# Kernel optimization log

Measured on AMD Instinct MI355X. Metric: run time of the kernel, lower is better.

## Reference

```python
import jax, jax.numpy as jnp
import numpy as np

BS, N, C = 16, 128, 512
EPS = 1e-5


def setup_inputs() -> dict:
    key = jax.random.key(0)
    ks = jax.random.split(key, 6)
    x = jax.random.normal(ks[0], (BS, N, C), dtype=jnp.float32)
    y = jax.random.normal(ks[1], (BS, C), dtype=jnp.float32)
    # edge conv: Conv2d(2C -> 1, 1x1), init std sqrt(2/(1*1*1))
    conv_e_w = jax.random.normal(ks[2], (1, 2 * C), dtype=jnp.float32) * np.sqrt(2.0)
    conv_e_b = jnp.zeros((1,), dtype=jnp.float32)
    bn_e_g = jnp.ones((1,), dtype=jnp.float32)
    bn_e_b = jnp.zeros((1,), dtype=jnp.float32)
    bn_e_m = jnp.zeros((1,), dtype=jnp.float32)
    bn_e_v = jnp.ones((1,), dtype=jnp.float32)
    # feature conv: Conv2d(2C -> C, 1x1), init std sqrt(2/C)
    conv_f_w = jax.random.normal(ks[3], (C, 2 * C), dtype=jnp.float32) * np.sqrt(2.0 / C)
    conv_f_b = jnp.zeros((C,), dtype=jnp.float32)
    bn_f_g = jnp.ones((C,), dtype=jnp.float32)
    bn_f_b = jnp.zeros((C,), dtype=jnp.float32)
    bn_f_m = jnp.zeros((C,), dtype=jnp.float32)
    bn_f_v = jnp.ones((C,), dtype=jnp.float32)
    return {
        "x": x, "y": y,
        "conv_e_w": conv_e_w, "conv_e_b": conv_e_b,
        "bn_e_g": bn_e_g, "bn_e_b": bn_e_b, "bn_e_m": bn_e_m, "bn_e_v": bn_e_v,
        "conv_f_w": conv_f_w, "conv_f_b": conv_f_b,
        "bn_f_g": bn_f_g, "bn_f_b": bn_f_b, "bn_f_m": bn_f_m, "bn_f_v": bn_f_v,
    }


def reference(x, y, conv_e_w, conv_e_b, bn_e_g, bn_e_b, bn_e_m, bn_e_v,
              conv_f_w, conv_f_b, bn_f_g, bn_f_b, bn_f_m, bn_f_v):
    bs, n, c = x.shape
    # ---- Wcompute: pairwise |x_i - x_j| -> conv1x1(2C->1) + BN + mask + softmax ----
    diff = jnp.abs(x[:, :, None, :] - x[:, None, :, :])  # [bs, N, N, C]
    w_diff = conv_e_w[0, :c]   # weights on pairwise-diff channels
    w_y = conv_e_w[0, c:]      # weights on broadcast y channels
    # 1x1 conv collapses to einsum; y part is constant over (i, j)
    score = (jnp.einsum('bijc,c->bij', diff, w_diff)
             + (y @ w_y)[:, None, None] + conv_e_b[0])  # [bs, N, N]
    # BatchNorm2d(1), inference mode
    score = (score - bn_e_m[0]) * (bn_e_g[0] * jax.lax.rsqrt(bn_e_v[0] + EPS)) + bn_e_b[0]
    # mask diagonal (W_id * 1e8) then softmax over neighbors j
    score = score - jnp.eye(n, dtype=score.dtype)[None] * 1e8
    W = jax.nn.softmax(score, axis=2)  # [bs, N, N]
    # ---- Gconv: neighbor aggregation + conv1x1(2C->C) + BN + ReLU ----
    x_nb = jnp.einsum('bij,bjc->bic', W, x)       # [bs, N, C]
    h = jnp.concatenate([x, x_nb], axis=2)        # [bs, N, 2C]
    out = jnp.einsum('bnk,ck->bnc', h, conv_f_w) + conv_f_b  # [bs, N, C]
    # BatchNorm2d(C), inference mode (per-channel)
    out = (out - bn_f_m) * (bn_f_g * jax.lax.rsqrt(bn_f_v + EPS)) + bn_f_b
    return jax.nn.relu(out)
```

## Files before the change

### kernel.cpp

```cpp
#include <hip/hip_runtime.h>
#include <hip/hip_bf16.h>

#define NTOK 128
#define CHN  512
#define KTOT 1024
#define EPSV 1e-5f

typedef __attribute__((ext_vector_type(8))) short bf16x8;
typedef __attribute__((ext_vector_type(4))) float f32x4;

union BfPack4 { ushort4 u; __hip_bfloat16 h[4]; };


__global__ __launch_bounds__(256)
void k0_transpose(const float* __restrict__ xg,
                  float* __restrict__ xT,
                  __hip_bfloat16* __restrict__ xTbf,
                  __hip_bfloat16* __restrict__ hb)
{
    __shared__ float ts[64 * 68];
    const int t  = threadIdx.x;
    const int bk = blockIdx.x;
    const int b  = bk >> 4;
    const int jt = (bk >> 3) & 1;
    const int ct = bk & 7;
    const int j0 = jt * 64, c0 = ct * 64;

    const int jr = t >> 2, qd = t & 3;
    const float* src = xg + ((size_t)(b * NTOK) + j0 + jr) * CHN + c0 + qd * 16;
    float4 v0 = *(const float4*)&src[0];
    float4 v1 = *(const float4*)&src[4];
    float4 v2 = *(const float4*)&src[8];
    float4 v3 = *(const float4*)&src[12];
    *(float4*)&ts[jr * 68 + qd * 16 + 0]  = v0;
    *(float4*)&ts[jr * 68 + qd * 16 + 4]  = v1;
    *(float4*)&ts[jr * 68 + qd * 16 + 8]  = v2;
    *(float4*)&ts[jr * 68 + qd * 16 + 12] = v3;

    {
        __hip_bfloat16* hrow = hb + ((size_t)(b * NTOK) + j0 + jr) * KTOT + c0 + qd * 16;
        BfPack4 p;
        p.h[0]=__float2bfloat16(v0.x); p.h[1]=__float2bfloat16(v0.y);
        p.h[2]=__float2bfloat16(v0.z); p.h[3]=__float2bfloat16(v0.w);
        *(ushort4*)&hrow[0] = p.u;
        p.h[0]=__float2bfloat16(v1.x); p.h[1]=__float2bfloat16(v1.y);
        p.h[2]=__float2bfloat16(v1.z); p.h[3]=__float2bfloat16(v1.w);
        *(ushort4*)&hrow[4] = p.u;
        p.h[0]=__float2bfloat16(v2.x); p.h[1]=__float2bfloat16(v2.y);
        p.h[2]=__float2bfloat16(v2.z); p.h[3]=__float2bfloat16(v2.w);
        *(ushort4*)&hrow[8] = p.u;
        p.h[0]=__float2bfloat16(v3.x); p.h[1]=__float2bfloat16(v3.y);
        p.h[2]=__float2bfloat16(v3.z); p.h[3]=__float2bfloat16(v3.w);
        *(ushort4*)&hrow[12] = p.u;
    }
    __syncthreads();

    const int cs = t >> 4, jj = (t & 15) * 4;
    #pragma unroll
    for (int m = 0; m < 4; ++m) {
        const int c = cs + 16 * m;
        float4 o;
        o.x = ts[(jj + 0) * 68 + c];
        o.y = ts[(jj + 1) * 68 + c];
        o.z = ts[(jj + 2) * 68 + c];
        o.w = ts[(jj + 3) * 68 + c];
        const size_t base = ((size_t)(b * CHN) + c0 + c) * NTOK + j0 + jj;
        *(float4*)&xT[base] = o;
        BfPack4 p;
        p.h[0]=__float2bfloat16(o.x); p.h[1]=__float2bfloat16(o.y);
        p.h[2]=__float2bfloat16(o.z); p.h[3]=__float2bfloat16(o.w);
        *(ushort4*)&xTbf[base] = p.u;
    }
}

__global__ __launch_bounds__(128)
void k1a_scores(const float* __restrict__ xg,
                const float* __restrict__ xT,
                const float* __restrict__ wde,
                float* __restrict__ part)
{
    const int bk = blockIdx.x;
    const int s  = bk & 7;
    const int iq = (bk >> 3) & 31;
    const int b  = bk >> 8;
    const int i0 = iq * 4;
    const int c0 = s * 64;
    const int j  = threadIdx.x;

    const float* xtp = xT + ((size_t)(b * CHN) + c0) * NTOK + j;
    const float* xip = xg + ((size_t)(b * NTOK) + i0) * CHN + c0;

    float acc0 = 0.f, acc1 = 0.f, acc2 = 0.f, acc3 = 0.f;

    #pragma unroll 2
    for (int cc = 0; cc < 64; cc += 8) {
        float xj[8];
        #pragma unroll
        for (int k = 0; k < 8; ++k) xj[k] = xtp[(cc + k) * NTOK];
        #pragma unroll
        for (int k = 0; k < 8; ++k) {
            const int c = cc + k;
            const float wd  = wde[c0 + c];
            const float xi0 = xip[0 * CHN + c];
            const float xi1 = xip[1 * CHN + c];
            const float xi2 = xip[2 * CHN + c];
            const float xi3 = xip[3 * CHN + c];
            acc0 += fabsf(xi0 - xj[k]) * wd;
            acc1 += fabsf(xi1 - xj[k]) * wd;
            acc2 += fabsf(xi2 - xj[k]) * wd;
            acc3 += fabsf(xi3 - xj[k]) * wd;
        }
    }

    float* pp = part + ((size_t)s * 16 + b) * (NTOK * NTOK) + (size_t)i0 * NTOK + j;
    pp[0 * NTOK] = acc0;
    pp[1 * NTOK] = acc1;
    pp[2 * NTOK] = acc2;
    pp[3 * NTOK] = acc3;
}

__global__ __launch_bounds__(128)
void k1b_softmax(const float* __restrict__ part,
                 const float* __restrict__ bn_e_g,
                 const float* __restrict__ bn_e_v,
                 __hip_bfloat16* __restrict__ Wbf)
{
    const int bk = blockIdx.x;
    const int b  = bk >> 6;
    const int i  = (bk & 63) * 2 + (threadIdx.x >> 6);
    const int l  = threadIdx.x & 63;

    const float* pp = part + (size_t)(b * NTOK + i) * NTOK;
    float p1 = 0.f, p2 = 0.f;
    #pragma unroll
    for (int s = 0; s < 8; ++s) {
        p1 += pp[(size_t)s * 16 * NTOK * NTOK + l];
        p2 += pp[(size_t)s * 16 * NTOK * NTOK + l + 64];
    }
    const float sc = bn_e_g[0] * rsqrtf(bn_e_v[0] + EPSV);
    float l1 = p1 * sc - (l == i ? 1e8f : 0.f);
    float l2 = p2 * sc - (l + 64 == i ? 1e8f : 0.f);

    float m = fmaxf(l1, l2);
    #pragma unroll
    for (int off = 32; off > 0; off >>= 1) m = fmaxf(m, __shfl_xor(m, off));
    const float e1 = __expf(l1 - m);
    const float e2 = __expf(l2 - m);
    float ssum = e1 + e2;
    #pragma unroll
    for (int off = 32; off > 0; off >>= 1) ssum += __shfl_xor(ssum, off);
    const float inv = 1.f / ssum;

    __hip_bfloat16* wr = Wbf + (size_t)(b * NTOK + i) * NTOK;
    wr[l]      = __float2bfloat16(e1 * inv);
    wr[l + 64] = __float2bfloat16(e2 * inv);
}

__global__ __launch_bounds__(256)
void k1c_xnb(const __hip_bfloat16* __restrict__ Wbf,
             const __hip_bfloat16* __restrict__ xTbf,
             const float* __restrict__ wf,
             __hip_bfloat16* __restrict__ hb,
             __hip_bfloat16* __restrict__ wfb)
{
    const int bk = blockIdx.x;
    const int t  = threadIdx.x;

    {
        const float* wr = wf + (size_t)bk * KTOT;
        float4 u = *(const float4*)&wr[t * 4];
        BfPack4 p;
        p.h[0]=__float2bfloat16(u.x); p.h[1]=__float2bfloat16(u.y);
        p.h[2]=__float2bfloat16(u.z); p.h[3]=__float2bfloat16(u.w);
        *(ushort4*)&wfb[(size_t)bk * KTOT + t * 4] = p.u;
    }

    const int b  = bk >> 5;
    const int mt = (bk >> 3) & 3;
    const int ct = bk & 7;
    const int i0 = mt * 32, c0 = ct * 64;

    const int w    = t >> 6;
    const int lane = t & 63;
    const int wm   = w & 1;
    const int wn   = w >> 1;
    const int m16  = lane & 15;
    const int q    = lane >> 4;

    const short* A0 = (const short*)Wbf  + (size_t)(b * NTOK + i0 + wm * 16 + m16) * NTOK + q * 8;
    const short* B0 = (const short*)xTbf + ((size_t)(b * CHN) + c0 + wn * 32 + m16) * NTOK + q * 8;

    f32x4 acc0 = {0.f, 0.f, 0.f, 0.f};
    f32x4 acc1 = acc0;

    #pragma unroll
    for (int k0 = 0; k0 < NTOK; k0 += 32) {
        const bf16x8 a  = *(const bf16x8*)(A0 + k0);
        const bf16x8 b0 = *(const bf16x8*)(B0 + k0);
        const bf16x8 b1 = *(const bf16x8*)(B0 + 16 * NTOK + k0);
        acc0 = __builtin_amdgcn_mfma_f32_16x16x32_bf16(a, b0, acc0, 0, 0, 0);
        acc1 = __builtin_amdgcn_mfma_f32_16x16x32_bf16(a, b1, acc1, 0, 0, 0);
    }

    #pragma unroll
    for (int ni = 0; ni < 2; ++ni) {
        const int c = c0 + wn * 32 + ni * 16 + m16;
        const f32x4 ac = ni ? acc1 : acc0;
        #pragma unroll
        for (int r = 0; r < 4; ++r) {
            const int i = i0 + wm * 16 + q * 4 + r;
            hb[(size_t)(b * NTOK + i) * KTOT + CHN + c] = __float2bfloat16(ac[r]);
        }
    }
}

__global__ __launch_bounds__(256)
void k2_gemm_bn_relu(const __hip_bfloat16* __restrict__ hbp,
                     const __hip_bfloat16* __restrict__ wfbp,
                     const float* __restrict__ fb,
                     const float* __restrict__ gg,
                     const float* __restrict__ bb,
                     const float* __restrict__ mm,
                     const float* __restrict__ vv,
                     float* __restrict__ out)
{
    const int blk  = blockIdx.x;
    const int r0   = (blk >> 3) << 6;
    const int c0   = (blk & 7) << 6;
    const int t    = threadIdx.x;
    const int w    = t >> 6;
    const int lane = t & 63;
    const int wm   = w & 1;
    const int wn   = w >> 1;
    const int m16  = lane & 15;
    const int qq   = lane >> 4;

    const short* A0 = (const short*)hbp  + (size_t)(r0 + wm * 32 + m16) * KTOT + qq * 8;
    const short* B0 = (const short*)wfbp + (size_t)(c0 + wn * 32 + m16) * KTOT + qq * 8;

    f32x4 acc00 = {0.f, 0.f, 0.f, 0.f};
    f32x4 acc01 = acc00, acc10 = acc00, acc11 = acc00;

    #pragma unroll 4
    for (int k0 = 0; k0 < KTOT; k0 += 32) {
        const bf16x8 aA = *(const bf16x8*)(A0 + k0);
        const bf16x8 aB = *(const bf16x8*)(A0 + 16 * KTOT + k0);
        const bf16x8 bA = *(const bf16x8*)(B0 + k0);
        const bf16x8 bB = *(const bf16x8*)(B0 + 16 * KTOT + k0);
        acc00 = __builtin_amdgcn_mfma_f32_16x16x32_bf16(aA, bA, acc00, 0, 0, 0);
        acc01 = __builtin_amdgcn_mfma_f32_16x16x32_bf16(aA, bB, acc01, 0, 0, 0);
        acc10 = __builtin_amdgcn_mfma_f32_16x16x32_bf16(aB, bA, acc10, 0, 0, 0);
        acc11 = __builtin_amdgcn_mfma_f32_16x16x32_bf16(aB, bB, acc11, 0, 0, 0);
    }

    #pragma unroll
    for (int ni = 0; ni < 2; ++ni) {
        const int c = c0 + wn * 32 + ni * 16 + m16;
        const float gf = gg[c] * rsqrtf(vv[c] + EPSV);
        const float ad = fb[c] - mm[c];
        const float bv = bb[c];
        const f32x4 acr0 = ni ? acc01 : acc00;
        const f32x4 acr1 = ni ? acc11 : acc10;
        #pragma unroll
        for (int r2 = 0; r2 < 4; ++r2) {
            int row = r0 + wm * 32 + qq * 4 + r2;
            float val = (acr0[r2] + ad) * gf + bv;
            out[(size_t)row * CHN + c] = fmaxf(val, 0.f);
            row += 16;
            val = (acr1[r2] + ad) * gf + bv;
            out[(size_t)row * CHN + c] = fmaxf(val, 0.f);
        }
    }
}

extern "C" void kernel_launch(void* const* d_in, const int* in_sizes, int n_in,
                              void* d_out, int out_size, void* d_ws, size_t ws_size,
                              hipStream_t stream) {
    const float* x        = (const float*)d_in[0];
    const float* conv_e_w = (const float*)d_in[2];
    const float* bn_e_g   = (const float*)d_in[4];
    const float* bn_e_v   = (const float*)d_in[7];
    const float* conv_f_w = (const float*)d_in[8];
    const float* conv_f_b = (const float*)d_in[9];
    const float* bn_f_g   = (const float*)d_in[10];
    const float* bn_f_b   = (const float*)d_in[11];
    const float* bn_f_m   = (const float*)d_in[12];
    const float* bn_f_v   = (const float*)d_in[13];
    float* out = (float*)d_out;

    char* ws = (char*)d_ws;
    float*           xT   = (float*)(ws);
    float*           part = (float*)(ws + (4u << 20));
    __hip_bfloat16*  hb   = (__hip_bfloat16*)(ws + (12u << 20));
    __hip_bfloat16*  wfb  = (__hip_bfloat16*)(ws + (16u << 20));
    __hip_bfloat16*  Wbf  = (__hip_bfloat16*)(ws + (17u << 20));
    __hip_bfloat16*  xTbf = (__hip_bfloat16*)(ws + (17u << 20) + (512u << 10));

    k0_transpose<<<256, 256, 0, stream>>>(x, xT, xTbf, hb);
    k1a_scores<<<4096, 128, 0, stream>>>(x, xT, conv_e_w, part);
    k1b_softmax<<<1024, 128, 0, stream>>>(part, bn_e_g, bn_e_v, Wbf);
    k1c_xnb<<<512, 256, 0, stream>>>(Wbf, xTbf, conv_f_w, hb, wfb);
    k2_gemm_bn_relu<<<256, 256, 0, stream>>>(hb, wfb, conv_f_b, bn_f_g, bn_f_b,
                                             bn_f_m, bn_f_v, out);
}
```

Before: 123.1 us.

## Fuse softmax into neighbor GEMM and vectorize score kernel with channel-quad layout

The separate softmax kernel is merged into the neighbor-aggregation kernel. Each block reduces the partial scores for its 32 rows, computes the masked softmax and keeps the bf16 weights in shared memory instead of writing them to global memory and reading them back. The score kernel now processes 8 query rows per block and reads a new channel-quad interleaved transposed layout with float4 loads, which raises reuse per loaded x_j. In exchange, the fused kernel recomputes the softmax once per channel tile (8x redundant), and the transpose kernel now writes the bf16 transpose with scalar stores.

```diff
diff --git a/kernel.cpp b/kernel.cpp
--- a/kernel.cpp
+++ b/kernel.cpp
@@ -14,7 +14,7 @@
 
 __global__ __launch_bounds__(256)
 void k0_transpose(const float* __restrict__ xg,
-                  float* __restrict__ xT,
+                  float* __restrict__ xT4,
                   __hip_bfloat16* __restrict__ xTbf,
                   __hip_bfloat16* __restrict__ hb)
 {
@@ -55,114 +55,69 @@
     }
     __syncthreads();
 
-    const int cs = t >> 4, jj = (t & 15) * 4;
+    const int jr2 = t & 63;
     #pragma unroll
     for (int m = 0; m < 4; ++m) {
-        const int c = cs + 16 * m;
-        float4 o;
-        o.x = ts[(jj + 0) * 68 + c];
-        o.y = ts[(jj + 1) * 68 + c];
-        o.z = ts[(jj + 2) * 68 + c];
-        o.w = ts[(jj + 3) * 68 + c];
-        const size_t base = ((size_t)(b * CHN) + c0 + c) * NTOK + j0 + jj;
-        *(float4*)&xT[base] = o;
-        BfPack4 p;
-        p.h[0]=__float2bfloat16(o.x); p.h[1]=__float2bfloat16(o.y);
-        p.h[2]=__float2bfloat16(o.z); p.h[3]=__float2bfloat16(o.w);
-        *(ushort4*)&xTbf[base] = p.u;
+        const int cg = (t >> 6) * 4 + m;
+        float4 f4 = *(const float4*)&ts[jr2 * 68 + cg * 4];
+        const size_t slot = ((size_t)(b * 128) + (c0 >> 2) + cg) * NTOK + j0 + jr2;
+        *(float4*)&xT4[slot * 4] = f4;
+        const int c = c0 + cg * 4;
+        xTbf[((size_t)(b * CHN) + c + 0) * NTOK + j0 + jr2] = __float2bfloat16(f4.x);
+        xTbf[((size_t)(b * CHN) + c + 1) * NTOK + j0 + jr2] = __float2bfloat16(f4.y);
+        xTbf[((size_t)(b * CHN) + c + 2) * NTOK + j0 + jr2] = __float2bfloat16(f4.z);
+        xTbf[((size_t)(b * CHN) + c + 3) * NTOK + j0 + jr2] = __float2bfloat16(f4.w);
     }
 }
 
 __global__ __launch_bounds__(128)
 void k1a_scores(const float* __restrict__ xg,
-                const float* __restrict__ xT,
+                const float* __restrict__ xT4,
                 const float* __restrict__ wde,
                 float* __restrict__ part)
 {
     const int bk = blockIdx.x;
     const int s  = bk & 7;
-    const int iq = (bk >> 3) & 31;
-    const int b  = bk >> 8;
-    const int i0 = iq * 4;
+    const int iq = (bk >> 3) & 15;
+    const int b  = bk >> 7;
+    const int i0 = iq * 8;
     const int c0 = s * 64;
     const int j  = threadIdx.x;
 
-    const float* xtp = xT + ((size_t)(b * CHN) + c0) * NTOK + j;
+    const float* xt  = xT4 + ((size_t)(b * 128 + s * 16) * NTOK + j) * 4;
     const float* xip = xg + ((size_t)(b * NTOK) + i0) * CHN + c0;
 
-    float acc0 = 0.f, acc1 = 0.f, acc2 = 0.f, acc3 = 0.f;
-
-    #pragma unroll 2
-    for (int cc = 0; cc < 64; cc += 8) {
-        float xj[8];
-        #pragma unroll
-        for (int k = 0; k < 8; ++k) xj[k] = xtp[(cc + k) * NTOK];
-        #pragma unroll
-        for (int k = 0; k < 8; ++k) {
-            const int c = cc + k;
-            const float wd  = wde[c0 + c];
-            const float xi0 = xip[0 * CHN + c];
-            const float xi1 = xip[1 * CHN + c];
-            const float xi2 = xip[2 * CHN + c];
-            const float xi3 = xip[3 * CHN + c];
-            acc0 += fabsf(xi0 - xj[k]) * wd;
-            acc1 += fabsf(xi1 - xj[k]) * wd;
-            acc2 += fabsf(xi2 - xj[k]) * wd;
-            acc3 += fabsf(xi3 - xj[k]) * wd;
-        }
-    }
-
-    float* pp = part + ((size_t)s * 16 + b) * (NTOK * NTOK) + (size_t)i0 * NTOK + j;
-    pp[0 * NTOK] = acc0;
-    pp[1 * NTOK] = acc1;
-    pp[2 * NTOK] = acc2;
-    pp[3 * NTOK] = acc3;
-}
-
-__global__ __launch_bounds__(128)
-void k1b_softmax(const float* __restrict__ part,
-                 const float* __restrict__ bn_e_g,
-                 const float* __restrict__ bn_e_v,
-                 __hip_bfloat16* __restrict__ Wbf)
+    float acc[8];
+    #pragma unroll
+    for (int r = 0; r < 8; ++r) acc[r] = 0.f;
+
+    #pragma unroll 4
+    for (int g = 0; g < 16; ++g) {
+        const float4 xj = *(const float4*)(xt + (size_t)g * NTOK * 4);
+        const float4 wd = *(const float4*)&wde[c0 + g * 4];
+        #pragma unroll
+        for (int r = 0; r < 8; ++r) {
+            const float4 xi = *(const float4*)&xip[r * CHN + g * 4];
+            acc[r] += fabsf(xi.x - xj.x) * wd.x + fabsf(xi.y - xj.y) * wd.y
+                    + fabsf(xi.z - xj.z) * wd.z + fabsf(xi.w - xj.w) * wd.w;
+        }
+    }
+
+    float* pp = part + ((size_t)(s * 16 + b)) * (NTOK * NTOK) + (size_t)i0 * NTOK + j;
+    #pragma unroll
+    for (int r = 0; r < 8; ++r) pp[r * NTOK] = acc[r];
+}
+
+__global__ __launch_bounds__(256)
+void k1bc_softmax_xnb(const float* __restrict__ part,
+                      const float* __restrict__ bn_e_g,
+                      const float* __restrict__ bn_e_v,
+                      const __hip_bfloat16* __restrict__ xTbf,
+                      const float* __restrict__ wf,
+                      __hip_bfloat16* __restrict__ hb,
+                      __hip_bfloat16* __restrict__ wfb)
 {
-    const int bk = blockIdx.x;
-    const int b  = bk >> 6;
-    const int i  = (bk & 63) * 2 + (threadIdx.x >> 6);
-    const int l  = threadIdx.x & 63;
-
-    const float* pp = part + (size_t)(b * NTOK + i) * NTOK;
-    float p1 = 0.f, p2 = 0.f;
-    #pragma unroll
-    for (int s = 0; s < 8; ++s) {
-        p1 += pp[(size_t)s * 16 * NTOK * NTOK + l];
-        p2 += pp[(size_t)s * 16 * NTOK * NTOK + l + 64];
-    }
-    const float sc = bn_e_g[0] * rsqrtf(bn_e_v[0] + EPSV);
-    float l1 = p1 * sc - (l == i ? 1e8f : 0.f);
-    float l2 = p2 * sc - (l + 64 == i ? 1e8f : 0.f);
-
-    float m = fmaxf(l1, l2);
-    #pragma unroll
-    for (int off = 32; off > 0; off >>= 1) m = fmaxf(m, __shfl_xor(m, off));
-    const float e1 = __expf(l1 - m);
-    const float e2 = __expf(l2 - m);
-    float ssum = e1 + e2;
-    #pragma unroll
-    for (int off = 32; off > 0; off >>= 1) ssum += __shfl_xor(ssum, off);
-    const float inv = 1.f / ssum;
-
-    __hip_bfloat16* wr = Wbf + (size_t)(b * NTOK + i) * NTOK;
-    wr[l]      = __float2bfloat16(e1 * inv);
-    wr[l + 64] = __float2bfloat16(e2 * inv);
-}
-
-__global__ __launch_bounds__(256)
-void k1c_xnb(const __hip_bfloat16* __restrict__ Wbf,
-             const __hip_bfloat16* __restrict__ xTbf,
-             const float* __restrict__ wf,
-             __hip_bfloat16* __restrict__ hb,
-             __hip_bfloat16* __restrict__ wfb)
-{
+    __shared__ unsigned short WL[32 * 128];
     const int bk = blockIdx.x;
     const int t  = threadIdx.x;
 
@@ -180,6 +135,57 @@
     const int ct = bk & 7;
     const int i0 = mt * 32, c0 = ct * 64;
 
+    {
+        const int r    = t >> 3;
+        const int jseg = (t & 7) * 16;
+        const int gi   = i0 + r;
+
+        float4 s0 = {0,0,0,0}, s1 = s0, s2 = s0, s3 = s0;
+        #pragma unroll
+        for (int s = 0; s < 8; ++s) {
+            const float* pp = part + ((size_t)(s * 16 + b)) * (NTOK * NTOK)
+                            + (size_t)gi * NTOK + jseg;
+            float4 a = *(const float4*)&pp[0];
+            float4 bq = *(const float4*)&pp[4];
+            float4 cq = *(const float4*)&pp[8];
+            float4 dq = *(const float4*)&pp[12];
+            s0.x+=a.x; s0.y+=a.y; s0.z+=a.z; s0.w+=a.w;
+            s1.x+=bq.x; s1.y+=bq.y; s1.z+=bq.z; s1.w+=bq.w;
+            s2.x+=cq.x; s2.y+=cq.y; s2.z+=cq.z; s2.w+=cq.w;
+            s3.x+=dq.x; s3.y+=dq.y; s3.z+=dq.z; s3.w+=dq.w;
+        }
+        const float sc = bn_e_g[0] * rsqrtf(bn_e_v[0] + EPSV);
+        float l[16] = { s0.x,s0.y,s0.z,s0.w, s1.x,s1.y,s1.z,s1.w,
+                        s2.x,s2.y,s2.z,s2.w, s3.x,s3.y,s3.z,s3.w };
+        #pragma unroll
+        for (int k = 0; k < 16; ++k) l[k] *= sc;
+        if (gi >= jseg && gi < jseg + 16) l[gi - jseg] -= 1e8f;
+
+        float m = l[0];
+        #pragma unroll
+        for (int k = 1; k < 16; ++k) m = fmaxf(m, l[k]);
+        m = fmaxf(m, __shfl_xor(m, 1));
+        m = fmaxf(m, __shfl_xor(m, 2));
+        m = fmaxf(m, __shfl_xor(m, 4));
+        float e[16], ssum = 0.f;
+        #pragma unroll
+        for (int k = 0; k < 16; ++k) { e[k] = __expf(l[k] - m); ssum += e[k]; }
+        ssum += __shfl_xor(ssum, 1);
+        ssum += __shfl_xor(ssum, 2);
+        ssum += __shfl_xor(ssum, 4);
+        const float inv = 1.f / ssum;
+        #pragma unroll
+        for (int k4 = 0; k4 < 4; ++k4) {
+            BfPack4 p;
+            p.h[0] = __float2bfloat16(e[k4*4+0] * inv);
+            p.h[1] = __float2bfloat16(e[k4*4+1] * inv);
+            p.h[2] = __float2bfloat16(e[k4*4+2] * inv);
+            p.h[3] = __float2bfloat16(e[k4*4+3] * inv);
+            *(ushort4*)&WL[r * 128 + jseg + k4 * 4] = p.u;
+        }
+    }
+    __syncthreads();
+
     const int w    = t >> 6;
     const int lane = t & 63;
     const int wm   = w & 1;
@@ -187,7 +193,7 @@
     const int m16  = lane & 15;
     const int q    = lane >> 4;
 
-    const short* A0 = (const short*)Wbf  + (size_t)(b * NTOK + i0 + wm * 16 + m16) * NTOK + q * 8;
+    const unsigned short* A0 = &WL[(wm * 16 + m16) * 128 + q * 8];
     const short* B0 = (const short*)xTbf + ((size_t)(b * CHN) + c0 + wn * 32 + m16) * NTOK + q * 8;
 
     f32x4 acc0 = {0.f, 0.f, 0.f, 0.f};
@@ -289,17 +295,16 @@
     float* out = (float*)d_out;
 
     char* ws = (char*)d_ws;
-    float*           xT   = (float*)(ws);
-    float*           part = (float*)(ws + (4u << 20));
+    float*           xT4  = (float*)(ws);
+    float*           part = (float*)(ws + (4u  << 20));
     __hip_bfloat16*  hb   = (__hip_bfloat16*)(ws + (12u << 20));
     __hip_bfloat16*  wfb  = (__hip_bfloat16*)(ws + (16u << 20));
-    __hip_bfloat16*  Wbf  = (__hip_bfloat16*)(ws + (17u << 20));
-    __hip_bfloat16*  xTbf = (__hip_bfloat16*)(ws + (17u << 20) + (512u << 10));
-
-    k0_transpose<<<256, 256, 0, stream>>>(x, xT, xTbf, hb);
-    k1a_scores<<<4096, 128, 0, stream>>>(x, xT, conv_e_w, part);
-    k1b_softmax<<<1024, 128, 0, stream>>>(part, bn_e_g, bn_e_v, Wbf);
-    k1c_xnb<<<512, 256, 0, stream>>>(Wbf, xTbf, conv_f_w, hb, wfb);
+    __hip_bfloat16*  xTbf = (__hip_bfloat16*)(ws + (17u << 20));
+
+    k0_transpose<<<256, 256, 0, stream>>>(x, xT4, xTbf, hb);
+    k1a_scores<<<2048, 128, 0, stream>>>(x, xT4, conv_e_w, part);
+    k1bc_softmax_xnb<<<512, 256, 0, stream>>>(part, bn_e_g, bn_e_v, xTbf,
+                                              conv_f_w, hb, wfb);
     k2_gemm_bn_relu<<<256, 256, 0, stream>>>(hb, wfb, conv_f_b, bn_f_g, bn_f_b,
                                              bn_f_m, bn_f_v, out);
 }
```

New measurement: 138.4 us. 1.12x slower.

## Fuse neighbor aggregation into final GEMM and stage x tile in LDS for scores

Applied to the files above, without the earlier changes.

The scores kernel now loads a per-batch x channel slice into shared memory, transposed in place, instead of reading a global fp32 transpose. It also computes 8 rows per 256-thread block. The xT fp32 buffer and the separate x_nb kernel are removed. The final kernel recomputes W·x for its 64-row tile into LDS, then runs the concat GEMM from bf16 x and that LDS buffer. This removes one launch and the hb round trip, at the cost of redundant W·x work across the 8 column-tile blocks.

```diff
diff --git a/kernel.cpp b/kernel.cpp
--- a/kernel.cpp
+++ b/kernel.cpp
@@ -5,6 +5,7 @@
 #define CHN  512
 #define KTOT 1024
 #define EPSV 1e-5f
+#define XNB_LD 520
 
 typedef __attribute__((ext_vector_type(8))) short bf16x8;
 typedef __attribute__((ext_vector_type(4))) float f32x4;
@@ -13,10 +14,72 @@
 
 
 __global__ __launch_bounds__(256)
-void k0_transpose(const float* __restrict__ xg,
-                  float* __restrict__ xT,
-                  __hip_bfloat16* __restrict__ xTbf,
-                  __hip_bfloat16* __restrict__ hb)
+void k1a_scores(const float* __restrict__ xg,
+                const float* __restrict__ wde,
+                float* __restrict__ part)
+{
+    __shared__ float xs[64 * 129];
+    const int bk = blockIdx.x;
+    const int s  = bk & 7;
+    const int ib = (bk >> 3) & 15;
+    const int b  = bk >> 7;
+    const int i0 = ib * 8;
+    const int c0 = s * 64;
+    const int t  = threadIdx.x;
+    const float* __restrict__ xb = xg + (size_t)b * NTOK * CHN;
+
+    const int cq = t & 15, jb = t >> 4;
+    #pragma unroll
+    for (int u = 0; u < 8; ++u) {
+        const int j = jb + 16 * u;
+        float4 v = *(const float4*)&xb[(size_t)j * CHN + c0 + cq * 4];
+        xs[(cq * 4 + 0) * 129 + j] = v.x;
+        xs[(cq * 4 + 1) * 129 + j] = v.y;
+        xs[(cq * 4 + 2) * 129 + j] = v.z;
+        xs[(cq * 4 + 3) * 129 + j] = v.w;
+    }
+    __syncthreads();
+
+    const int j  = t & 127;
+    const int rh = t >> 7;
+    const float* xip = xb + (size_t)(i0 + rh * 4) * CHN + c0;
+
+    float acc[4] = {0.f, 0.f, 0.f, 0.f};
+    #pragma unroll 4
+    for (int g = 0; g < 16; ++g) {
+        const float4 wd  = *(const float4*)&wde[c0 + g * 4];
+        const float4 xi0 = *(const float4*)&xip[0 * CHN + g * 4];
+        const float4 xi1 = *(const float4*)&xip[1 * CHN + g * 4];
+        const float4 xi2 = *(const float4*)&xip[2 * CHN + g * 4];
+        const float4 xi3 = *(const float4*)&xip[3 * CHN + g * 4];
+        const float xj0 = xs[(g * 4 + 0) * 129 + j];
+        const float xj1 = xs[(g * 4 + 1) * 129 + j];
+        const float xj2 = xs[(g * 4 + 2) * 129 + j];
+        const float xj3 = xs[(g * 4 + 3) * 129 + j];
+        acc[0] += fabsf(xi0.x - xj0) * wd.x + fabsf(xi0.y - xj1) * wd.y
+                + fabsf(xi0.z - xj2) * wd.z + fabsf(xi0.w - xj3) * wd.w;
+        acc[1] += fabsf(xi1.x - xj0) * wd.x + fabsf(xi1.y - xj1) * wd.y
+                + fabsf(xi1.z - xj2) * wd.z + fabsf(xi1.w - xj3) * wd.w;
+        acc[2] += fabsf(xi2.x - xj0) * wd.x + fabsf(xi2.y - xj1) * wd.y
+                + fabsf(xi2.z - xj2) * wd.z + fabsf(xi2.w - xj3) * wd.w;
+        acc[3] += fabsf(xi3.x - xj0) * wd.x + fabsf(xi3.y - xj1) * wd.y
+                + fabsf(xi3.z - xj2) * wd.z + fabsf(xi3.w - xj3) * wd.w;
+    }
+
+    float* pp = part + ((size_t)s * 16 + b) * (NTOK * NTOK)
+              + (size_t)(i0 + rh * 4) * NTOK + j;
+    pp[0 * NTOK] = acc[0];
+    pp[1 * NTOK] = acc[1];
+    pp[2 * NTOK] = acc[2];
+    pp[3 * NTOK] = acc[3];
+}
+
+__global__ __launch_bounds__(256)
+void k0_prep(const float* __restrict__ xg,
+             const float* __restrict__ wf,
+             __hip_bfloat16* __restrict__ xbf,
+             __hip_bfloat16* __restrict__ xTbf,
+             __hip_bfloat16* __restrict__ wfb)
 {
     __shared__ float ts[64 * 68];
     const int t  = threadIdx.x;
@@ -25,6 +88,20 @@
     const int jt = (bk >> 3) & 1;
     const int ct = bk & 7;
     const int j0 = jt * 64, c0 = ct * 64;
+
+    {
+        const float* wr = wf + (size_t)(2 * bk) * KTOT;
+        __hip_bfloat16* wo = wfb + (size_t)(2 * bk) * KTOT;
+        #pragma unroll
+        for (int u = 0; u < 2; ++u) {
+            const int idx = t + u * 256;
+            float4 v = *(const float4*)&wr[idx * 4];
+            BfPack4 p;
+            p.h[0]=__float2bfloat16(v.x); p.h[1]=__float2bfloat16(v.y);
+            p.h[2]=__float2bfloat16(v.z); p.h[3]=__float2bfloat16(v.w);
+            *(ushort4*)&wo[idx * 4] = p.u;
+        }
+    }
 
     const int jr = t >> 2, qd = t & 3;
     const float* src = xg + ((size_t)(b * NTOK) + j0 + jr) * CHN + c0 + qd * 16;
@@ -38,7 +115,7 @@
     *(float4*)&ts[jr * 68 + qd * 16 + 12] = v3;
 
     {
-        __hip_bfloat16* hrow = hb + ((size_t)(b * NTOK) + j0 + jr) * KTOT + c0 + qd * 16;
+        __hip_bfloat16* hrow = xbf + ((size_t)(b * NTOK) + j0 + jr) * CHN + c0 + qd * 16;
         BfPack4 p;
         p.h[0]=__float2bfloat16(v0.x); p.h[1]=__float2bfloat16(v0.y);
         p.h[2]=__float2bfloat16(v0.z); p.h[3]=__float2bfloat16(v0.w);
@@ -59,64 +136,13 @@
     #pragma unroll
     for (int m = 0; m < 4; ++m) {
         const int c = cs + 16 * m;
-        float4 o;
-        o.x = ts[(jj + 0) * 68 + c];
-        o.y = ts[(jj + 1) * 68 + c];
-        o.z = ts[(jj + 2) * 68 + c];
-        o.w = ts[(jj + 3) * 68 + c];
-        const size_t base = ((size_t)(b * CHN) + c0 + c) * NTOK + j0 + jj;
-        *(float4*)&xT[base] = o;
         BfPack4 p;
-        p.h[0]=__float2bfloat16(o.x); p.h[1]=__float2bfloat16(o.y);
-        p.h[2]=__float2bfloat16(o.z); p.h[3]=__float2bfloat16(o.w);
-        *(ushort4*)&xTbf[base] = p.u;
-    }
-}
-
-__global__ __launch_bounds__(128)
-void k1a_scores(const float* __restrict__ xg,
-                const float* __restrict__ xT,
-                const float* __restrict__ wde,
-                float* __restrict__ part)
-{
-    const int bk = blockIdx.x;
-    const int s  = bk & 7;
-    const int iq = (bk >> 3) & 31;
-    const int b  = bk >> 8;
-    const int i0 = iq * 4;
-    const int c0 = s * 64;
-    const int j  = threadIdx.x;
-
-    const float* xtp = xT + ((size_t)(b * CHN) + c0) * NTOK + j;
-    const float* xip = xg + ((size_t)(b * NTOK) + i0) * CHN + c0;
-
-    float acc0 = 0.f, acc1 = 0.f, acc2 = 0.f, acc3 = 0.f;
-
-    #pragma unroll 2
-    for (int cc = 0; cc < 64; cc += 8) {
-        float xj[8];
-        #pragma unroll
-        for (int k = 0; k < 8; ++k) xj[k] = xtp[(cc + k) * NTOK];
-        #pragma unroll
-        for (int k = 0; k < 8; ++k) {
-            const int c = cc + k;
-            const float wd  = wde[c0 + c];
-            const float xi0 = xip[0 * CHN + c];
-            const float xi1 = xip[1 * CHN + c];
-            const float xi2 = xip[2 * CHN + c];
-            const float xi3 = xip[3 * CHN + c];
-            acc0 += fabsf(xi0 - xj[k]) * wd;
-            acc1 += fabsf(xi1 - xj[k]) * wd;
-            acc2 += fabsf(xi2 - xj[k]) * wd;
-            acc3 += fabsf(xi3 - xj[k]) * wd;
-        }
-    }
-
-    float* pp = part + ((size_t)s * 16 + b) * (NTOK * NTOK) + (size_t)i0 * NTOK + j;
-    pp[0 * NTOK] = acc0;
-    pp[1 * NTOK] = acc1;
-    pp[2 * NTOK] = acc2;
-    pp[3 * NTOK] = acc3;
+        p.h[0] = __float2bfloat16(ts[(jj + 0) * 68 + c]);
+        p.h[1] = __float2bfloat16(ts[(jj + 1) * 68 + c]);
+        p.h[2] = __float2bfloat16(ts[(jj + 2) * 68 + c]);
+        p.h[3] = __float2bfloat16(ts[(jj + 3) * 68 + c]);
+        *(ushort4*)&xTbf[((size_t)(b * CHN) + c0 + c) * NTOK + j0 + jj] = p.u;
+    }
 }
 
 __global__ __launch_bounds__(128)
@@ -157,96 +183,90 @@
 }
 
 __global__ __launch_bounds__(256)
-void k1c_xnb(const __hip_bfloat16* __restrict__ Wbf,
-             const __hip_bfloat16* __restrict__ xTbf,
-             const float* __restrict__ wf,
-             __hip_bfloat16* __restrict__ hb,
-             __hip_bfloat16* __restrict__ wfb)
+void k2_fused(const __hip_bfloat16* __restrict__ Wbf,
+              const __hip_bfloat16* __restrict__ xTbf,
+              const __hip_bfloat16* __restrict__ xbf,
+              const __hip_bfloat16* __restrict__ wfb,
+              const float* __restrict__ fb,
+              const float* __restrict__ gg,
+              const float* __restrict__ bb,
+              const float* __restrict__ mm,
+              const float* __restrict__ vv,
+              float* __restrict__ out)
 {
-    const int bk = blockIdx.x;
-    const int t  = threadIdx.x;
-
-    {
-        const float* wr = wf + (size_t)bk * KTOT;
-        float4 u = *(const float4*)&wr[t * 4];
-        BfPack4 p;
-        p.h[0]=__float2bfloat16(u.x); p.h[1]=__float2bfloat16(u.y);
-        p.h[2]=__float2bfloat16(u.z); p.h[3]=__float2bfloat16(u.w);
-        *(ushort4*)&wfb[(size_t)bk * KTOT + t * 4] = p.u;
-    }
-
-    const int b  = bk >> 5;
-    const int mt = (bk >> 3) & 3;
-    const int ct = bk & 7;
-    const int i0 = mt * 32, c0 = ct * 64;
-
-    const int w    = t >> 6;
-    const int lane = t & 63;
-    const int wm   = w & 1;
-    const int wn   = w >> 1;
-    const int m16  = lane & 15;
-    const int q    = lane >> 4;
-
-    const short* A0 = (const short*)Wbf  + (size_t)(b * NTOK + i0 + wm * 16 + m16) * NTOK + q * 8;
-    const short* B0 = (const short*)xTbf + ((size_t)(b * CHN) + c0 + wn * 32 + m16) * NTOK + q * 8;
-
-    f32x4 acc0 = {0.f, 0.f, 0.f, 0.f};
-    f32x4 acc1 = acc0;
-
-    #pragma unroll
-    for (int k0 = 0; k0 < NTOK; k0 += 32) {
-        const bf16x8 a  = *(const bf16x8*)(A0 + k0);
-        const bf16x8 b0 = *(const bf16x8*)(B0 + k0);
-        const bf16x8 b1 = *(const bf16x8*)(B0 + 16 * NTOK + k0);
-        acc0 = __builtin_amdgcn_mfma_f32_16x16x32_bf16(a, b0, acc0, 0, 0, 0);
-        acc1 = __builtin_amdgcn_mfma_f32_16x16x32_bf16(a, b1, acc1, 0, 0, 0);
-    }
-
-    #pragma unroll
-    for (int ni = 0; ni < 2; ++ni) {
-        const int c = c0 + wn * 32 + ni * 16 + m16;
-        const f32x4 ac = ni ? acc1 : acc0;
-        #pragma unroll
-        for (int r = 0; r < 4; ++r) {
-            const int i = i0 + wm * 16 + q * 4 + r;
-            hb[(size_t)(b * NTOK + i) * KTOT + CHN + c] = __float2bfloat16(ac[r]);
-        }
-    }
-}
-
-__global__ __launch_bounds__(256)
-void k2_gemm_bn_relu(const __hip_bfloat16* __restrict__ hbp,
-                     const __hip_bfloat16* __restrict__ wfbp,
-                     const float* __restrict__ fb,
-                     const float* __restrict__ gg,
-                     const float* __restrict__ bb,
-                     const float* __restrict__ mm,
-                     const float* __restrict__ vv,
-                     float* __restrict__ out)
-{
-    const int blk  = blockIdx.x;
-    const int r0   = (blk >> 3) << 6;
-    const int c0   = (blk & 7) << 6;
+    __shared__ unsigned short xnb[64 * XNB_LD];
+    const int blk = blockIdx.x;
+    const int rt  = blk >> 3;
+    const int ct  = blk & 7;
+    const int b   = rt >> 1;
+    const int i0  = (rt & 1) * 64;
+    const int c0  = ct * 64;
     const int t    = threadIdx.x;
     const int w    = t >> 6;
     const int lane = t & 63;
-    const int wm   = w & 1;
-    const int wn   = w >> 1;
     const int m16  = lane & 15;
-    const int qq   = lane >> 4;
-
-    const short* A0 = (const short*)hbp  + (size_t)(r0 + wm * 32 + m16) * KTOT + qq * 8;
-    const short* B0 = (const short*)wfbp + (size_t)(c0 + wn * 32 + m16) * KTOT + qq * 8;
+    const int q    = lane >> 4;
+
+    {
+        const int n0w = w * 128;
+        #pragma unroll
+        for (int mt = 0; mt < 4; ++mt) {
+            const short* Ar = (const short*)Wbf
+                            + (size_t)(b * NTOK + i0 + mt * 16 + m16) * NTOK + q * 8;
+            const bf16x8 a0 = *(const bf16x8*)(Ar + 0);
+            const bf16x8 a1 = *(const bf16x8*)(Ar + 32);
+            const bf16x8 a2 = *(const bf16x8*)(Ar + 64);
+            const bf16x8 a3 = *(const bf16x8*)(Ar + 96);
+            #pragma unroll
+            for (int nt = 0; nt < 8; ++nt) {
+                const int n = n0w + nt * 16;
+                const short* Br = (const short*)xTbf
+                                + ((size_t)(b * CHN) + n + m16) * NTOK + q * 8;
+                f32x4 acc = {0.f, 0.f, 0.f, 0.f};
+                acc = __builtin_amdgcn_mfma_f32_16x16x32_bf16(a0, *(const bf16x8*)(Br + 0),  acc, 0, 0, 0);
+                acc = __builtin_amdgcn_mfma_f32_16x16x32_bf16(a1, *(const bf16x8*)(Br + 32), acc, 0, 0, 0);
+                acc = __builtin_amdgcn_mfma_f32_16x16x32_bf16(a2, *(const bf16x8*)(Br + 64), acc, 0, 0, 0);
+                acc = __builtin_amdgcn_mfma_f32_16x16x32_bf16(a3, *(const bf16x8*)(Br + 96), acc, 0, 0, 0);
+                #pragma unroll
+                for (int r = 0; r < 4; ++r) {
+                    __hip_bfloat16 hv = __float2bfloat16(acc[r]);
+                    xnb[(mt * 16 + q * 4 + r) * XNB_LD + n + m16] =
+                        *(unsigned short*)&hv;
+                }
+            }
+        }
+    }
+    __syncthreads();
+
+    const int wm = w & 1;
+    const int wn = w >> 1;
+
+    const short* AL = (const short*)xbf
+                    + (size_t)(b * NTOK + i0 + wm * 32 + m16) * CHN + q * 8;
+    const short* BW = (const short*)wfb
+                    + (size_t)(c0 + wn * 32 + m16) * KTOT + q * 8;
+    const unsigned short* AR = &xnb[(wm * 32 + m16) * XNB_LD + q * 8];
 
     f32x4 acc00 = {0.f, 0.f, 0.f, 0.f};
     f32x4 acc01 = acc00, acc10 = acc00, acc11 = acc00;
 
     #pragma unroll 4
-    for (int k0 = 0; k0 < KTOT; k0 += 32) {
-        const bf16x8 aA = *(const bf16x8*)(A0 + k0);
-        const bf16x8 aB = *(const bf16x8*)(A0 + 16 * KTOT + k0);
-        const bf16x8 bA = *(const bf16x8*)(B0 + k0);
-        const bf16x8 bB = *(const bf16x8*)(B0 + 16 * KTOT + k0);
+    for (int k0 = 0; k0 < 512; k0 += 32) {
+        const bf16x8 aA = *(const bf16x8*)(AL + k0);
+        const bf16x8 aB = *(const bf16x8*)(AL + 16 * CHN + k0);
+        const bf16x8 bA = *(const bf16x8*)(BW + k0);
+        const bf16x8 bB = *(const bf16x8*)(BW + 16 * KTOT + k0);
+        acc00 = __builtin_amdgcn_mfma_f32_16x16x32_bf16(aA, bA, acc00, 0, 0, 0);
+        acc01 = __builtin_amdgcn_mfma_f32_16x16x32_bf16(aA, bB, acc01, 0, 0, 0);
+        acc10 = __builtin_amdgcn_mfma_f32_16x16x32_bf16(aB, bA, acc10, 0, 0, 0);
+        acc11 = __builtin_amdgcn_mfma_f32_16x16x32_bf16(aB, bB, acc11, 0, 0, 0);
+    }
+    #pragma unroll 4
+    for (int k0 = 0; k0 < 512; k0 += 32) {
+        const bf16x8 aA = *(const bf16x8*)(AR + k0);
+        const bf16x8 aB = *(const bf16x8*)(AR + 16 * XNB_LD + k0);
+        const bf16x8 bA = *(const bf16x8*)(BW + 512 + k0);
+        const bf16x8 bB = *(const bf16x8*)(BW + 16 * KTOT + 512 + k0);
         acc00 = __builtin_amdgcn_mfma_f32_16x16x32_bf16(aA, bA, acc00, 0, 0, 0);
         acc01 = __builtin_amdgcn_mfma_f32_16x16x32_bf16(aA, bB, acc01, 0, 0, 0);
         acc10 = __builtin_amdgcn_mfma_f32_16x16x32_bf16(aB, bA, acc10, 0, 0, 0);
@@ -263,7 +283,7 @@
         const f32x4 acr1 = ni ? acc11 : acc10;
         #pragma unroll
         for (int r2 = 0; r2 < 4; ++r2) {
-            int row = r0 + wm * 32 + qq * 4 + r2;
+            int row = b * NTOK + i0 + wm * 32 + q * 4 + r2;
             float val = (acr0[r2] + ad) * gf + bv;
             out[(size_t)row * CHN + c] = fmaxf(val, 0.f);
             row += 16;
@@ -289,17 +309,15 @@
     float* out = (float*)d_out;
 
     char* ws = (char*)d_ws;
-    float*           xT   = (float*)(ws);
-    float*           part = (float*)(ws + (4u << 20));
-    __hip_bfloat16*  hb   = (__hip_bfloat16*)(ws + (12u << 20));
-    __hip_bfloat16*  wfb  = (__hip_bfloat16*)(ws + (16u << 20));
-    __hip_bfloat16*  Wbf  = (__hip_bfloat16*)(ws + (17u << 20));
-    __hip_bfloat16*  xTbf = (__hip_bfloat16*)(ws + (17u << 20) + (512u << 10));
-
-    k0_transpose<<<256, 256, 0, stream>>>(x, xT, xTbf, hb);
-    k1a_scores<<<4096, 128, 0, stream>>>(x, xT, conv_e_w, part);
+    float*          part = (float*)(ws);
+    __hip_bfloat16* Wbf  = (__hip_bfloat16*)(ws + (8u << 20));
+    __hip_bfloat16* xTbf = (__hip_bfloat16*)(ws + (8u << 20) + (512u << 10));
+    __hip_bfloat16* xbf  = (__hip_bfloat16*)(ws + (10u << 20) + (512u << 10));
+    __hip_bfloat16* wfb  = (__hip_bfloat16*)(ws + (12u << 20) + (512u << 10));
+
+    k1a_scores<<<2048, 256, 0, stream>>>(x, conv_e_w, part);
+    k0_prep<<<256, 256, 0, stream>>>(x, conv_f_w, xbf, xTbf, wfb);
     k1b_softmax<<<1024, 128, 0, stream>>>(part, bn_e_g, bn_e_v, Wbf);
-    k1c_xnb<<<512, 256, 0, stream>>>(Wbf, xTbf, conv_f_w, hb, wfb);
-    k2_gemm_bn_relu<<<256, 256, 0, stream>>>(hb, wfb, conv_f_b, bn_f_g, bn_f_b,
-                                             bn_f_m, bn_f_v, out);
-}
+    k2_fused<<<256, 256, 0, stream>>>(Wbf, xTbf, xbf, wfb, conv_f_b,
+                                      bn_f_g, bn_f_b, bn_f_m, bn_f_v, out);
+}
```

Measured after the change: 139.7 us. +13.5%, slower.
